# Optimization experiments

Measured on AMD Instinct MI355X. Metric: run time of the kernel, lower is better.

The kernel has to match this reference:

```python
import jax, jax.numpy as jnp
import numpy as np

N_CLASSES = 8  # hardcoded by the (-1, 8, 8) reshape in the original layer

def setup_inputs() -> dict:
    key = jax.random.key(0)
    k1, k2, k3, k4 = jax.random.split(key, 4)
    B, F, C, R = 16384, 128, N_CLASSES, 64
    x = jax.random.normal(k1, (B, F), dtype=jnp.float32)
    p = jax.random.uniform(k2, (B, C), dtype=jnp.float32)  # class-prob-like input
    W = jax.random.normal(k3, (F, C * C, R), dtype=jnp.float32) * 0.02
    b = jax.random.normal(k4, (C, C, R), dtype=jnp.float32) * 0.1
    return {"x": x, "p": p, "W": W, "b": b}

def reference(x, p, W, b):
    # x: (B, 128) features; p: (B, C) class probs; W: (128, C*C, R); b: (C, C, R)
    B = x.shape[0]
    C = b.shape[0]
    R = b.shape[-1]
    # per-annotator GEMM fused across all annotators: (B, C*C, R)
    logits = jnp.einsum('bf,fkr->bkr', x, W).reshape(B, C, C, R) + b[None]
    # row-softmax: softmax over the "predicted class" axis for each true class c
    M = jax.nn.softmax(logits, axis=2)  # (B, C, C, R)
    # batched dot: p (B,C) contracted against rows of each annotator matrix
    out = jnp.einsum('bc,bcdr->bdr', p, M)  # (B, C, R)
    # NOTE: original applies K.dropout(0.5) (training-mode); omitted for a
    # deterministic inference reference (identity at eval).
    return out
```

## Files before the change

### kernel.cpp

```cpp
#include <hip/hip_runtime.h>
#include <hip/hip_bf16.h>


#define B_ROWS   16384
#define F_DIM    128
#define NCOL     4096
#define OUT_STRIDE 512
#define LOG2E    1.44269504088896340736f

typedef __bf16 bf16x8 __attribute__((ext_vector_type(8)));
typedef float  f32x4  __attribute__((ext_vector_type(4)));

#define AS1(p) ((const __attribute__((address_space(1))) unsigned int*)(p))
#define AS3(p) ((__attribute__((address_space(3))) unsigned int*)(p))

__global__ void wconv_kernel(const float* __restrict__ W, __bf16* __restrict__ wf) {
    int f    = blockIdx.x * 256 + threadIdx.x;
    int lane = f & 63;
    int tkk  = f >> 6;
    int t    = tkk >> 2;
    int kk   = tkk & 3;
    int kbase = kk * 32 + (lane >> 4) * 8;
    int n     = t * 16 + (lane & 15);
    bf16x8 frag;
    for (int j = 0; j < 8; ++j)
        frag[j] = (__bf16)W[(kbase + j) * NCOL + n];
    *(bf16x8*)(wf + f * 8) = frag;
}

__global__ __launch_bounds__(256, 4)
void fused_kernel(const float* __restrict__ x, const float* __restrict__ p,
                  const float* __restrict__ bias, const __bf16* __restrict__ wf,
                  float* __restrict__ out) {
    __shared__ __align__(16) char lds[32768];

    const int lane = threadIdx.x & 63;
    const int ww   = threadIdx.x >> 6;
    const int quad = lane >> 4;
    const int l15  = lane & 15;
    const int w    = blockIdx.x & 3;
    const int b0   = (blockIdx.x >> 2) * 64 + ww * 16;

    bf16x8 afr[4];
    {
        const float* xr = x + (b0 + l15) * F_DIM + quad * 8;
#pragma unroll
        for (int kk = 0; kk < 4; ++kk) {
            float4 lo = *(const float4*)(xr + kk * 32);
            float4 hi = *(const float4*)(xr + kk * 32 + 4);
            bf16x8 f;
            f[0] = (__bf16)lo.x; f[1] = (__bf16)lo.y;
            f[2] = (__bf16)lo.z; f[3] = (__bf16)lo.w;
            f[4] = (__bf16)hi.x; f[5] = (__bf16)hi.y;
            f[6] = (__bf16)hi.z; f[7] = (__bf16)hi.w;
            afr[kk] = f;
        }
    }

    float O[8][4] = {};

#pragma unroll 1
    for (int c = 0; c < 8; ++c) {
        {
#pragma unroll
            for (int j = 0; j < 8; ++j) {
                int d  = ww * 2 + (j >> 2);
                int kk = j & 3;
                int gf = ((c * 8 + d) * 4 + w) * 4 + kk;
                __builtin_amdgcn_global_load_lds(
                    AS1(wf + (size_t)gf * 512 + lane * 8),
                    AS3(lds + (d * 4 + kk) * 1024), 16, 0, 0);
            }
        }
        __syncthreads();

        float pvv[4];
#pragma unroll
        for (int jj = 0; jj < 4; ++jj)
            pvv[jj] = p[(b0 + quad * 4 + jj) * 8 + c];

        float bvl[8];
#pragma unroll
        for (int d = 0; d < 8; ++d)
            bvl[d] = bias[(c * 8 + d) * 64 + w * 16 + l15] * LOG2E;

        f32x4 acc[8] = {};
#pragma unroll
        for (int kk = 0; kk < 4; ++kk)
#pragma unroll
            for (int d = 0; d < 8; ++d) {
                bf16x8 bfr = *(const bf16x8*)(lds + (d * 4 + kk) * 1024 + lane * 16);
                acc[d] = __builtin_amdgcn_mfma_f32_16x16x32_bf16(
                             afr[kk], bfr, acc[d], 0, 0, 0);
            }

#pragma unroll
        for (int jj = 0; jj < 4; ++jj) {
            float e[8];
#pragma unroll
            for (int d = 0; d < 8; ++d)
                e[d] = __builtin_amdgcn_exp2f(
                           __builtin_fmaf(acc[d][jj], LOG2E, bvl[d]));
            float s01 = e[0] + e[1], s23 = e[2] + e[3];
            float s45 = e[4] + e[5], s67 = e[6] + e[7];
            float s = (s01 + s23) + (s45 + s67);
            float scale = pvv[jj] * __builtin_amdgcn_rcpf(s);
#pragma unroll
            for (int d = 0; d < 8; ++d)
                O[d][jj] = __builtin_fmaf(e[d], scale, O[d][jj]);
        }
        __syncthreads();
    }

#pragma unroll
    for (int jj = 0; jj < 4; ++jj) {
        float* orow = out + (b0 + quad * 4 + jj) * OUT_STRIDE + w * 16 + l15;
#pragma unroll
        for (int d = 0; d < 8; ++d)
            orow[d * 64] = O[d][jj];
    }
}

extern "C" void kernel_launch(void* const* d_in, const int* in_sizes, int n_in,
                              void* d_out, int out_size, void* d_ws, size_t ws_size,
                              hipStream_t stream) {
    const float* x    = (const float*)d_in[0];
    const float* p    = (const float*)d_in[1];
    const float* W    = (const float*)d_in[2];
    const float* bias = (const float*)d_in[3];
    float* out = (float*)d_out;
    __bf16* wf = (__bf16*)d_ws;

    wconv_kernel<<<dim3(256), dim3(256), 0, stream>>>(W, wf);
    fused_kernel<<<dim3(1024), dim3(256), 0, stream>>>(x, p, bias, wf, out);
}
```

Before: 105.7 us.

## Switch to 32x32x16 MFMA with swapped operands and LDS-staged coalesced output stores

Reorganizes the fused GEMM+softmax kernel to use 32x32x16 bf16 MFMA, with the weight tile as the A operand and x as the B operand. The weight fragments are reordered so that each lane's accumulator holds all 8 softmax classes for a row locally. A separate kernel pre-permutes the bias and pre-scales it by log2e so it can be read as float4 vectors. Outputs are transposed through LDS so the global stores are contiguous 16-byte writes instead of strided scalar stores. This adds an extra small kernel launch and more accumulator registers in exchange for fewer MFMA instructions and better store coalescing.

```diff
diff --git a/kernel.cpp b/kernel.cpp
--- a/kernel.cpp
+++ b/kernel.cpp
@@ -2,122 +2,160 @@
 #include <hip/hip_bf16.h>
 
 
-#define B_ROWS   16384
-#define F_DIM    128
-#define NCOL     4096
-#define OUT_STRIDE 512
-#define LOG2E    1.44269504088896340736f
+#define LOG2E 1.44269504088896340736f
 
 typedef __bf16 bf16x8 __attribute__((ext_vector_type(8)));
 typedef float  f32x4  __attribute__((ext_vector_type(4)));
+typedef float  f32x16 __attribute__((ext_vector_type(16)));
 
 #define AS1(p) ((const __attribute__((address_space(1))) unsigned int*)(p))
 #define AS3(p) ((__attribute__((address_space(3))) unsigned int*)(p))
 
+
 __global__ void wconv_kernel(const float* __restrict__ W, __bf16* __restrict__ wf) {
     int f    = blockIdx.x * 256 + threadIdx.x;
     int lane = f & 63;
-    int tkk  = f >> 6;
-    int t    = tkk >> 2;
-    int kk   = tkk & 3;
-    int kbase = kk * 32 + (lane >> 4) * 8;
-    int n     = t * 16 + (lane & 15);
+    int g    = f >> 6;
+    int kq   = g & 7;
+    int rg   = (g >> 3) & 15;
+    int c    = g >> 7;
+    int rho  = lane & 31;
+    int kh   = lane >> 5;
+    int d    = (rho & 3) | ((rho >> 1) & 4);
+    int rr   = ((rho >> 2) & 1) | ((rho >> 3) & 2);
+    int n    = (c * 8 + d) * 64 + rg * 4 + rr;
+    int kbase = kq * 16 + kh * 8;
     bf16x8 frag;
     for (int j = 0; j < 8; ++j)
-        frag[j] = (__bf16)W[(kbase + j) * NCOL + n];
+        frag[j] = (__bf16)W[(kbase + j) * 4096 + n];
     *(bf16x8*)(wf + f * 8) = frag;
+}
+
+__global__ void bconv_kernel(const float* __restrict__ bias, float* __restrict__ bs) {
+    int t  = blockIdx.x * 256 + threadIdx.x;
+    int jj = t & 15;
+    int h  = (t >> 4) & 1;
+    int c  = (t >> 5) & 7;
+    int rg = t >> 8;
+    int d  = jj & 7;
+    int r  = rg * 4 + h + 2 * (jj >> 3);
+    bs[t] = bias[(c * 8 + d) * 64 + r] * LOG2E;
 }
 
 __global__ __launch_bounds__(256, 4)
 void fused_kernel(const float* __restrict__ x, const float* __restrict__ p,
-                  const float* __restrict__ bias, const __bf16* __restrict__ wf,
+                  const float* __restrict__ bs, const __bf16* __restrict__ wf,
                   float* __restrict__ out) {
     __shared__ __align__(16) char lds[32768];
 
     const int lane = threadIdx.x & 63;
     const int ww   = threadIdx.x >> 6;
-    const int quad = lane >> 4;
-    const int l15  = lane & 15;
-    const int w    = blockIdx.x & 3;
-    const int b0   = (blockIdx.x >> 2) * 64 + ww * 16;
+    const int l31  = lane & 31;
+    const int h    = lane >> 5;
+    const int rp   = blockIdx.x & 3;
+    const int b0   = (blockIdx.x >> 2) * 64;
+    const int bw   = b0 + (ww & 1) * 32;
+    const int rgp  = ww >> 1;
 
-    bf16x8 afr[4];
+    bf16x8 bfr[8];
     {
-        const float* xr = x + (b0 + l15) * F_DIM + quad * 8;
+        const float* xr = x + (bw + l31) * 128 + h * 8;
 #pragma unroll
-        for (int kk = 0; kk < 4; ++kk) {
-            float4 lo = *(const float4*)(xr + kk * 32);
-            float4 hi = *(const float4*)(xr + kk * 32 + 4);
-            bf16x8 f;
-            f[0] = (__bf16)lo.x; f[1] = (__bf16)lo.y;
-            f[2] = (__bf16)lo.z; f[3] = (__bf16)lo.w;
-            f[4] = (__bf16)hi.x; f[5] = (__bf16)hi.y;
-            f[6] = (__bf16)hi.z; f[7] = (__bf16)hi.w;
-            afr[kk] = f;
+        for (int kq = 0; kq < 8; ++kq) {
+            float4 lo = *(const float4*)(xr + kq * 16);
+            float4 hi = *(const float4*)(xr + kq * 16 + 4);
+            bf16x8 fr;
+            fr[0] = (__bf16)lo.x; fr[1] = (__bf16)lo.y;
+            fr[2] = (__bf16)lo.z; fr[3] = (__bf16)lo.w;
+            fr[4] = (__bf16)hi.x; fr[5] = (__bf16)hi.y;
+            fr[6] = (__bf16)hi.z; fr[7] = (__bf16)hi.w;
+            bfr[kq] = fr;
         }
     }
 
-    float O[8][4] = {};
+    float O0[16], O1[16];
+#pragma unroll
+    for (int z = 0; z < 16; ++z) { O0[z] = 0.f; O1[z] = 0.f; }
 
 #pragma unroll 1
     for (int c = 0; c < 8; ++c) {
         {
+            const __bf16* g = wf + (size_t)((c * 16 + rp * 4 + ww) * 8) * 512 + lane * 8;
 #pragma unroll
-            for (int j = 0; j < 8; ++j) {
-                int d  = ww * 2 + (j >> 2);
-                int kk = j & 3;
-                int gf = ((c * 8 + d) * 4 + w) * 4 + kk;
-                __builtin_amdgcn_global_load_lds(
-                    AS1(wf + (size_t)gf * 512 + lane * 8),
-                    AS3(lds + (d * 4 + kk) * 1024), 16, 0, 0);
-            }
+            for (int kq = 0; kq < 8; ++kq)
+                __builtin_amdgcn_global_load_lds(AS1(g + kq * 512),
+                                                 AS3(lds + (ww * 8 + kq) * 1024), 16, 0, 0);
         }
         __syncthreads();
 
-        float pvv[4];
-#pragma unroll
-        for (int jj = 0; jj < 4; ++jj)
-            pvv[jj] = p[(b0 + quad * 4 + jj) * 8 + c];
-
-        float bvl[8];
-#pragma unroll
-        for (int d = 0; d < 8; ++d)
-            bvl[d] = bias[(c * 8 + d) * 64 + w * 16 + l15] * LOG2E;
-
-        f32x4 acc[8] = {};
-#pragma unroll
-        for (int kk = 0; kk < 4; ++kk)
-#pragma unroll
-            for (int d = 0; d < 8; ++d) {
-                bf16x8 bfr = *(const bf16x8*)(lds + (d * 4 + kk) * 1024 + lane * 16);
-                acc[d] = __builtin_amdgcn_mfma_f32_16x16x32_bf16(
-                             afr[kk], bfr, acc[d], 0, 0, 0);
-            }
+        float pv = p[(bw + l31) * 8 + c];
 
 #pragma unroll
-        for (int jj = 0; jj < 4; ++jj) {
-            float e[8];
+        for (int tt = 0; tt < 2; ++tt) {
+            const int rgl = rgp * 2 + tt;
+            f32x16 acc;
 #pragma unroll
-            for (int d = 0; d < 8; ++d)
-                e[d] = __builtin_amdgcn_exp2f(
-                           __builtin_fmaf(acc[d][jj], LOG2E, bvl[d]));
-            float s01 = e[0] + e[1], s23 = e[2] + e[3];
-            float s45 = e[4] + e[5], s67 = e[6] + e[7];
-            float s = (s01 + s23) + (s45 + s67);
-            float scale = pvv[jj] * __builtin_amdgcn_rcpf(s);
+            for (int z = 0; z < 16; ++z) acc[z] = 0.f;
 #pragma unroll
-            for (int d = 0; d < 8; ++d)
-                O[d][jj] = __builtin_fmaf(e[d], scale, O[d][jj]);
+            for (int kq = 0; kq < 8; ++kq) {
+                bf16x8 a = *(const bf16x8*)(lds + (rgl * 8 + kq) * 1024 + lane * 16);
+                acc = __builtin_amdgcn_mfma_f32_32x32x16_bf16(a, bfr[kq], acc, 0, 0, 0);
+            }
+            const float* bb = bs + (rp * 4 + rgl) * 256 + c * 32 + h * 16;
+            float4 bv0 = *(const float4*)(bb);
+            float4 bv1 = *(const float4*)(bb + 4);
+            float4 bv2 = *(const float4*)(bb + 8);
+            float4 bv3 = *(const float4*)(bb + 12);
+            float bv[16] = {bv0.x, bv0.y, bv0.z, bv0.w, bv1.x, bv1.y, bv1.z, bv1.w,
+                            bv2.x, bv2.y, bv2.z, bv2.w, bv3.x, bv3.y, bv3.z, bv3.w};
+            float* O = tt ? O1 : O0;
+#pragma unroll
+            for (int r3 = 0; r3 < 2; ++r3) {
+                float e[8];
+#pragma unroll
+                for (int dc = 0; dc < 8; ++dc)
+                    e[dc] = __builtin_amdgcn_exp2f(
+                        __builtin_fmaf(acc[r3 * 8 + dc], LOG2E, bv[r3 * 8 + dc]));
+                float s = ((e[0] + e[1]) + (e[2] + e[3])) + ((e[4] + e[5]) + (e[6] + e[7]));
+                float scale = pv * __builtin_amdgcn_rcpf(s);
+#pragma unroll
+                for (int dc = 0; dc < 8; ++dc)
+                    O[r3 * 8 + dc] = __builtin_fmaf(e[dc], scale, O[r3 * 8 + dc]);
+            }
         }
         __syncthreads();
     }
 
+    float* ldsF = (float*)lds;
 #pragma unroll
-    for (int jj = 0; jj < 4; ++jj) {
-        float* orow = out + (b0 + quad * 4 + jj) * OUT_STRIDE + w * 16 + l15;
+    for (int tt = 0; tt < 2; ++tt) {
+        const float* O = tt ? O1 : O0;
+        const int rbase = (rgp * 2 + tt) * 4 + h;
+        const int bl = (ww & 1) * 32 + l31;
 #pragma unroll
-        for (int d = 0; d < 8; ++d)
-            orow[d * 64] = O[d][jj];
+        for (int jj = 0; jj < 16; ++jj) {
+            int d  = jj & 7;
+            int rl = rbase + 2 * (jj >> 3);
+            ldsF[(d * 16 + rl) * 64 + bl] = O[jj];
+        }
+    }
+    __syncthreads();
+    const int q = threadIdx.x;
+#pragma unroll
+    for (int li = 0; li < 2; ++li) {
+        int ln = q + li * 256;
+        int bl = ln & 63;
+        int d  = ln >> 6;
+        float v[16];
+#pragma unroll
+        for (int k = 0; k < 16; ++k)
+            v[k] = ldsF[(d * 16 + k) * 64 + bl];
+        float* dst = out + (size_t)(b0 + bl) * 512 + d * 64 + rp * 16;
+#pragma unroll
+        for (int ch = 0; ch < 4; ++ch) {
+            f32x4 vv = {v[ch * 4], v[ch * 4 + 1], v[ch * 4 + 2], v[ch * 4 + 3]};
+            *(f32x4*)(dst + ch * 4) = vv;
+        }
     }
 }
 
@@ -130,7 +168,9 @@
     const float* bias = (const float*)d_in[3];
     float* out = (float*)d_out;
     __bf16* wf = (__bf16*)d_ws;
+    float*  bs = (float*)((char*)d_ws + (1 << 20));
 
     wconv_kernel<<<dim3(256), dim3(256), 0, stream>>>(W, wf);
-    fused_kernel<<<dim3(1024), dim3(256), 0, stream>>>(x, p, bias, wf, out);
+    bconv_kernel<<<dim3(16), dim3(256), 0, stream>>>(bias, bs);
+    fused_kernel<<<dim3(1024), dim3(256), 0, stream>>>(x, p, bs, wf, out);
 }
```

Result: slower. 114.1 us (+7.9%).
